# Optimization experiments

Hardware: AMD Instinct MI355X
Metric: run time of the kernel (lower is better)

## Reference

```python
import jax, jax.numpy as jnp
import numpy as np

HID = 256
N_LAYERS = 4
DT = 0.05
EPS = 1e-3
TMAX = 50


def setup_inputs() -> dict:
    key = jax.random.key(0)
    ks = jax.random.split(key, 7)
    B, S, D = 8, 1024, HID
    s1 = 1.0 / np.sqrt(D)      # fan_in = D for w_state / w_input
    s2 = 1.0 / np.sqrt(2 * D)  # fan_in = 2D for tau_gate linear
    x = jax.random.normal(ks[0], (B, S, D), dtype=jnp.float32)
    Ws = jax.random.uniform(ks[1], (N_LAYERS, D, D), jnp.float32, -s1, s1)
    bs = jax.random.uniform(ks[2], (N_LAYERS, D), jnp.float32, -s1, s1)
    Wi = jax.random.uniform(ks[3], (N_LAYERS, D, D), jnp.float32, -s1, s1)
    bi = jax.random.uniform(ks[4], (N_LAYERS, D), jnp.float32, -s1, s1)
    Wt = jax.random.uniform(ks[5], (N_LAYERS, D, 2 * D), jnp.float32, -s2, s2)
    bt = jax.random.uniform(ks[6], (N_LAYERS, D), jnp.float32, -s2, s2)
    return {"x": x, "Ws": Ws, "bs": bs, "Wi": Wi, "bi": bi, "Wt": Wt, "bt": bt}


def _run(x, Ws, bs, Wi, bi, Wt, bt):
    B, S, D = x.shape

    def layer_fn(cur_in, layer):
        h_prev, Ws_i, bs_i, Wi_i, bi_i, Wt_i, bt_i = layer
        combined = jnp.concatenate([cur_in, h_prev], axis=-1)          # [B,S,2D]
        tau = jax.nn.sigmoid(jnp.einsum('bsk,dk->bsd', combined, Wt_i) + bt_i)
        forcing = jnp.tanh(
            jnp.einsum('bsd,ed->bse', h_prev, Ws_i) + bs_i
            + jnp.einsum('bsd,ed->bse', cur_in, Wi_i) + bi_i
        )
        h_new = jnp.clip(h_prev + DT * (-h_prev / (tau + 1e-6) + forcing), -10.0, 10.0)
        delta = jnp.max(jnp.abs(h_new - h_prev))
        return h_new, (h_new, delta)

    @jax.checkpoint
    def step(carry, i):
        states, result, done = carry
        _, (new_states, deltas) = jax.lax.scan(
            layer_fn, x, (states, Ws, bs, Wi, bi, Wt, bt))
        converged = jnp.max(deltas) < EPS
        states = jnp.where(done, states, new_states)
        # torch returns loop index t at the first converging iteration, else TMAX
        result = jnp.where(done | ~converged, result, i)
        done = done | converged
        return (states, result, done), None

    init = (jnp.zeros((N_LAYERS, B, S, D), x.dtype),
            jnp.array(TMAX, jnp.int32),
            jnp.array(False))
    (states, result, _), _ = jax.lax.scan(step, init, jnp.arange(TMAX, dtype=jnp.int32))
    return states[-1], result


def reference(x, Ws, bs, Wi, bi, Wt, bt):
    return _run(x, Ws, bs, Wi, bi, Wt, bt)
```

## Files before the change

### kernel.cpp

```cpp
#include <hip/hip_runtime.h>
#include <math.h>

#define HID 256
#define TWOH 512
#define ROWS 8192
#define NLAYER 4
#define TMAX 50
#define DT 0.05f
#define EPSC 1e-3f

typedef float f32x4 __attribute__((ext_vector_type(4)));
typedef long  long2v __attribute__((ext_vector_type(2)));
typedef unsigned char u8;

__device__ inline u8 f32_to_fp8(float v) {
    return (u8)(__builtin_amdgcn_cvt_pk_fp8_f32(v, v, 0, 0) & 0xff);
}
__device__ inline float fp8_to_f32(u8 b) {
    return __builtin_amdgcn_cvt_f32_fp8((int)b, 0);
}

__global__ void pack_w_kernel(const float* __restrict__ Ws,
                              const float* __restrict__ Wi,
                              const float* __restrict__ Wt,
                              u8* __restrict__ Wf) {
    int e = blockIdx.x * 256 + threadIdx.x;
    int j    = e & 7;
    int h    = (e >> 3) & 1;
    int lane = (e >> 4) & 63;
    int g    = (e >> 10) & 1;
    int ci   = (e >> 11) & 15;
    int wv   = (e >> 15) & 7;
    int L    = (e >> 18);
    int l15  = lane & 15;
    int quad = lane >> 4;
    int d = wv * 32 + h * 16 + l15;
    int k = ci * 32 + quad * 8 + j;
    float v;
    if (g == 0) {
        v = Wt[(size_t)L * HID * TWOH + (size_t)d * TWOH + k];
    } else {
        v = (k < HID) ? Wi[(size_t)L * HID * HID + (size_t)d * HID + k]
                      : Ws[(size_t)L * HID * HID + (size_t)d * HID + (k - HID)];
    }
    Wf[e] = f32_to_fp8(v);
}

__global__ void pack_b_kernel(const float* __restrict__ bs,
                              const float* __restrict__ bi,
                              const float* __restrict__ bt,
                              float* __restrict__ bp) {
    int idx = blockIdx.x * 256 + threadIdx.x;
    int L = idx / TWOH;
    int n = idx % TWOH;
    int d = n >> 1;
    bp[idx] = ((n & 1) == 0) ? bt[L * HID + d]
                             : (bs[L * HID + d] + bi[L * HID + d]);
}

__global__ __launch_bounds__(512, 1) void persistent_kernel(
    const float* __restrict__ x,
    const u8* __restrict__ Wf,
    const float* __restrict__ bp,
    float* __restrict__ deltas,
    float* __restrict__ out)
{
    __shared__ u8 sX[32 * 256];
    __shared__ u8 sH[2][NLAYER][32 * 256];
    __shared__ float2 sBias[NLAYER][256];

    const int tid  = threadIdx.x;
    const int lane = tid & 63;
    const int wv   = tid >> 6;
    const int l15  = lane & 15;
    const int quad = lane >> 4;
    const int w32  = wv * 32;
    const size_t rowbase = (size_t)blockIdx.x * 32;

    #pragma unroll
    for (int it = 0; it < 2; ++it) {
        int s = tid + it * 512;
        int r = s >> 5, seg = s & 31;
        const float* gx = x + (rowbase + r) * HID + seg * 8;
        float4 v0 = *(const float4*)gx;
        float4 v1 = *(const float4*)(gx + 4);
        int lo = __builtin_amdgcn_cvt_pk_fp8_f32(v0.x, v0.y, 0, 0);
        lo     = __builtin_amdgcn_cvt_pk_fp8_f32(v0.z, v0.w, lo, 1);
        int hi = __builtin_amdgcn_cvt_pk_fp8_f32(v1.x, v1.y, 0, 0);
        hi     = __builtin_amdgcn_cvt_pk_fp8_f32(v1.z, v1.w, hi, 1);
        long pk = ((long)(unsigned int)lo) | ((long)hi << 32);
        *(long*)&sX[r * 256 + (seg ^ r) * 8] = pk;
    }
    {
        long* hflat = (long*)&sH[0][0][0];
        #pragma unroll
        for (int it = 0; it < 16; ++it) hflat[tid + it * 512] = 0;
    }
    #pragma unroll
    for (int it = 0; it < 2; ++it) {
        int i = tid + it * 512;
        sBias[i >> 8][i & 255] = *(const float2*)(bp + (i >> 8) * TWOH + 2 * (i & 255));
    }

    __syncthreads();

    #pragma unroll 1
    for (int t = 0; t < TMAX; ++t) {
        const int rs = t & 1, ws = rs ^ 1;
        #pragma unroll 1
        for (int L = 0; L < NLAYER; ++L) {
            const u8* Ahi = &sH[rs][L][0];
            const u8* Alo = (L == 0) ? sX : &sH[ws][L - 1][0];
            u8*       Hout = &sH[ws][L][0];
            const u8* wb = Wf + ((size_t)(L * 8 + wv) << 15) + (size_t)lane * 16;

            f32x4 acc[2][4];
            #pragma unroll
            for (int mt = 0; mt < 2; ++mt)
                #pragma unroll
                for (int n = 0; n < 4; ++n)
                    acc[mt][n] = (f32x4){0.f, 0.f, 0.f, 0.f};

            long2v bb[4][2];
            #pragma unroll
            for (int pi = 0; pi < 4; ++pi)
                #pragma unroll
                for (int g = 0; g < 2; ++g)
                    bb[pi][g] = *(const long2v*)(wb + (size_t)(((8 + pi) * 2 + g) << 10));

            #pragma unroll
            for (int s = 0; s < 16; ++s) {
                const int ci = (s < 8) ? (s + 8) : (s - 8);
                const int p = s & 3;
                if (s == 8) __syncthreads();
                const u8* Asrc = (s < 8) ? Ahi : Alo;
                const int seg = (ci & 7) * 4 + quad;
                long a[2];
                #pragma unroll
                for (int mt = 0; mt < 2; ++mt) {
                    const int row = mt * 16 + l15;
                    a[mt] = *(const long*)&Asrc[row * 256 + (seg ^ row) * 8];
                }
                #pragma unroll
                for (int mt = 0; mt < 2; ++mt)
                    #pragma unroll
                    for (int n = 0; n < 4; ++n)
                        acc[mt][n] = __builtin_amdgcn_mfma_f32_16x16x32_fp8_fp8(
                            a[mt], bb[p][n >> 1][n & 1], acc[mt][n], 0, 0, 0);
                if (s + 4 < 16) {
                    const int nci = (s + 4 < 8) ? (s + 12) : (s - 4);
                    #pragma unroll
                    for (int g = 0; g < 2; ++g)
                        bb[p][g] = *(const long2v*)(wb + (size_t)((nci * 2 + g) << 10));
                }
            }

            float dmax = 0.0f;
            #pragma unroll
            for (int ntp = 0; ntp < 2; ++ntp) {
                const int d = w32 + ntp * 16 + l15;
                const float2 b2 = sBias[L][d];
                const int seg = d >> 3, dlow = d & 7;
                #pragma unroll
                for (int mt = 0; mt < 2; ++mt) {
                    #pragma unroll
                    for (int r = 0; r < 4; ++r) {
                        float tpre = acc[mt][ntp][r]     + b2.x;
                        float fpre = acc[mt][ntp + 2][r] + b2.y;
                        tpre = fminf(30.f, fmaxf(-30.f, tpre));
                        fpre = fminf(15.f, fmaxf(-15.f, fpre));
                        float u   = __expf(-tpre);
                        float den = 1.0f + 1e-6f + 1e-6f * u;
                        float rcp = __builtin_amdgcn_rcpf(den);
                        float e2  = __expf(2.0f * fpre);
                        float r2  = __builtin_amdgcn_rcpf(e2 + 1.0f);
                        float fo  = (e2 - 1.0f) * r2;
                        const int row = mt * 16 + quad * 4 + r;
                        const int idx = row * 256 + (seg ^ row) * 8 + dlow;
                        float h  = fp8_to_f32(Ahi[idx]);
                        float gq = h * (1.0f + u) * rcp;
                        float nv = h + DT * (fo - gq);
                        nv = fminf(10.0f, fmaxf(-10.0f, nv));
                        Hout[idx] = f32_to_fp8(nv);
                        dmax = fmaxf(dmax, fabsf(nv - h));
                    }
                }
            }
            if (L == NLAYER - 1) {
                #pragma unroll
                for (int off = 32; off > 0; off >>= 1)
                    dmax = fmaxf(dmax, __shfl_xor(dmax, off));
                if (lane == 0)
                    atomicMax((unsigned int*)(deltas + t), __float_as_uint(dmax));
            }
        }
    }

    __syncthreads();

    {
        const u8* fin = &sH[((TMAX - 1) & 1) ^ 1][NLAYER - 1][0];
        #pragma unroll
        for (int it = 0; it < 2; ++it) {
            int s = tid + it * 512;
            int r = s >> 5, seg = s & 31;
            long v = *(const long*)&fin[r * 256 + (seg ^ r) * 8];
            int lo = (int)(v & 0xffffffffl);
            int hi = (int)(v >> 32);
            float* go = out + (rowbase + r) * HID + seg * 8;
            float4 o0, o1;
            o0.x = __builtin_amdgcn_cvt_f32_fp8(lo, 0);
            o0.y = __builtin_amdgcn_cvt_f32_fp8(lo, 1);
            o0.z = __builtin_amdgcn_cvt_f32_fp8(lo, 2);
            o0.w = __builtin_amdgcn_cvt_f32_fp8(lo, 3);
            o1.x = __builtin_amdgcn_cvt_f32_fp8(hi, 0);
            o1.y = __builtin_amdgcn_cvt_f32_fp8(hi, 1);
            o1.z = __builtin_amdgcn_cvt_f32_fp8(hi, 2);
            o1.w = __builtin_amdgcn_cvt_f32_fp8(hi, 3);
            *(float4*)go = o0;
            *(float4*)(go + 4) = o1;
        }
    }
}

__global__ void result_kernel(const float* __restrict__ deltas,
                              float* __restrict__ out) {
    if (threadIdx.x == 0) {
        int res = TMAX;
        for (int t = 0; t < TMAX; ++t) {
            if (deltas[t] < EPSC) { res = t; break; }
        }
        out[(size_t)ROWS * HID] = (float)res;
    }
}

extern "C" void kernel_launch(void* const* d_in, const int* in_sizes, int n_in,
                              void* d_out, int out_size, void* d_ws, size_t ws_size,
                              hipStream_t stream) {
    const float* x  = (const float*)d_in[0];
    const float* Ws = (const float*)d_in[1];
    const float* bs = (const float*)d_in[2];
    const float* Wi = (const float*)d_in[3];
    const float* bi = (const float*)d_in[4];
    const float* Wt = (const float*)d_in[5];
    const float* bt = (const float*)d_in[6];
    float* out = (float*)d_out;

    char* p = (char*)d_ws;
    u8*    Wf     = (u8*)p;    p += (size_t)NLAYER * TWOH * TWOH;
    float* bp     = (float*)p; p += (size_t)NLAYER * TWOH * sizeof(float);
    float* deltas = (float*)p; p += 64 * sizeof(float);

    hipMemsetAsync(deltas, 0, 64 * sizeof(float), stream);
    pack_w_kernel<<<(NLAYER * TWOH * TWOH) / 256, 256, 0, stream>>>(Ws, Wi, Wt, Wf);
    pack_b_kernel<<<(NLAYER * TWOH) / 256, 256, 0, stream>>>(bs, bi, bt, bp);

    persistent_kernel<<<256, 512, 0, stream>>>(x, Wf, bp, deltas, out);
    result_kernel<<<1, 64, 0, stream>>>(deltas, out);
}
```

Measured before the change: 1.257 ms.

## Halve rows per block to 16 and launch twice as many blocks

Each persistent block now handles 16 rows instead of 32, so the launch has 512 blocks instead of 256 and each wave issues one M-tile of MFMAs instead of two. The goal is to fill more of the MI355X's CUs, since 256 blocks leaves many idle. In exchange, every block still streams the full fp8 weight set from global/L2 each layer and timestep, which doubles total weight traffic, and weight-load latency is amortised over half as many MFMAs.

```diff
diff --git a/kernel.cpp b/kernel.cpp
--- a/kernel.cpp
+++ b/kernel.cpp
@@ -8,6 +8,7 @@
 #define TMAX 50
 #define DT 0.05f
 #define EPSC 1e-3f
+#define BROW 16
 
 typedef float f32x4 __attribute__((ext_vector_type(4)));
 typedef long  long2v __attribute__((ext_vector_type(2)));
@@ -65,8 +66,8 @@
     float* __restrict__ deltas,
     float* __restrict__ out)
 {
-    __shared__ u8 sX[32 * 256];
-    __shared__ u8 sH[2][NLAYER][32 * 256];
+    __shared__ u8 sX[BROW * 256];
+    __shared__ u8 sH[2][NLAYER][BROW * 256];
     __shared__ float2 sBias[NLAYER][256];
 
     const int tid  = threadIdx.x;
@@ -75,12 +76,10 @@
     const int l15  = lane & 15;
     const int quad = lane >> 4;
     const int w32  = wv * 32;
-    const size_t rowbase = (size_t)blockIdx.x * 32;
-
-    #pragma unroll
-    for (int it = 0; it < 2; ++it) {
-        int s = tid + it * 512;
-        int r = s >> 5, seg = s & 31;
+    const size_t rowbase = (size_t)blockIdx.x * BROW;
+
+    {
+        int r = tid >> 5, seg = tid & 31;
         const float* gx = x + (rowbase + r) * HID + seg * 8;
         float4 v0 = *(const float4*)gx;
         float4 v1 = *(const float4*)(gx + 4);
@@ -94,7 +93,7 @@
     {
         long* hflat = (long*)&sH[0][0][0];
         #pragma unroll
-        for (int it = 0; it < 16; ++it) hflat[tid + it * 512] = 0;
+        for (int it = 0; it < 8; ++it) hflat[tid + it * 512] = 0;
     }
     #pragma unroll
     for (int it = 0; it < 2; ++it) {
@@ -114,12 +113,10 @@
             u8*       Hout = &sH[ws][L][0];
             const u8* wb = Wf + ((size_t)(L * 8 + wv) << 15) + (size_t)lane * 16;
 
-            f32x4 acc[2][4];
-            #pragma unroll
-            for (int mt = 0; mt < 2; ++mt)
-                #pragma unroll
-                for (int n = 0; n < 4; ++n)
-                    acc[mt][n] = (f32x4){0.f, 0.f, 0.f, 0.f};
+            f32x4 acc[4];
+            #pragma unroll
+            for (int n = 0; n < 4; ++n)
+                acc[n] = (f32x4){0.f, 0.f, 0.f, 0.f};
 
             long2v bb[4][2];
             #pragma unroll
@@ -135,18 +132,11 @@
                 if (s == 8) __syncthreads();
                 const u8* Asrc = (s < 8) ? Ahi : Alo;
                 const int seg = (ci & 7) * 4 + quad;
-                long a[2];
-                #pragma unroll
-                for (int mt = 0; mt < 2; ++mt) {
-                    const int row = mt * 16 + l15;
-                    a[mt] = *(const long*)&Asrc[row * 256 + (seg ^ row) * 8];
-                }
-                #pragma unroll
-                for (int mt = 0; mt < 2; ++mt)
-                    #pragma unroll
-                    for (int n = 0; n < 4; ++n)
-                        acc[mt][n] = __builtin_amdgcn_mfma_f32_16x16x32_fp8_fp8(
-                            a[mt], bb[p][n >> 1][n & 1], acc[mt][n], 0, 0, 0);
+                long a = *(const long*)&Asrc[l15 * 256 + (seg ^ l15) * 8];
+                #pragma unroll
+                for (int n = 0; n < 4; ++n)
+                    acc[n] = __builtin_amdgcn_mfma_f32_16x16x32_fp8_fp8(
+                        a, bb[p][n >> 1][n & 1], acc[n], 0, 0, 0);
                 if (s + 4 < 16) {
                     const int nci = (s + 4 < 8) ? (s + 12) : (s - 4);
                     #pragma unroll
@@ -162,28 +152,25 @@
                 const float2 b2 = sBias[L][d];
                 const int seg = d >> 3, dlow = d & 7;
                 #pragma unroll
-                for (int mt = 0; mt < 2; ++mt) {
-                    #pragma unroll
-                    for (int r = 0; r < 4; ++r) {
-                        float tpre = acc[mt][ntp][r]     + b2.x;
-                        float fpre = acc[mt][ntp + 2][r] + b2.y;
-                        tpre = fminf(30.f, fmaxf(-30.f, tpre));
-                        fpre = fminf(15.f, fmaxf(-15.f, fpre));
-                        float u   = __expf(-tpre);
-                        float den = 1.0f + 1e-6f + 1e-6f * u;
-                        float rcp = __builtin_amdgcn_rcpf(den);
-                        float e2  = __expf(2.0f * fpre);
-                        float r2  = __builtin_amdgcn_rcpf(e2 + 1.0f);
-                        float fo  = (e2 - 1.0f) * r2;
-                        const int row = mt * 16 + quad * 4 + r;
-                        const int idx = row * 256 + (seg ^ row) * 8 + dlow;
-                        float h  = fp8_to_f32(Ahi[idx]);
-                        float gq = h * (1.0f + u) * rcp;
-                        float nv = h + DT * (fo - gq);
-                        nv = fminf(10.0f, fmaxf(-10.0f, nv));
-                        Hout[idx] = f32_to_fp8(nv);
-                        dmax = fmaxf(dmax, fabsf(nv - h));
-                    }
+                for (int r = 0; r < 4; ++r) {
+                    float tpre = acc[ntp][r]     + b2.x;
+                    float fpre = acc[ntp + 2][r] + b2.y;
+                    tpre = fminf(30.f, fmaxf(-30.f, tpre));
+                    fpre = fminf(15.f, fmaxf(-15.f, fpre));
+                    float u   = __expf(-tpre);
+                    float den = 1.0f + 1e-6f + 1e-6f * u;
+                    float rcp = __builtin_amdgcn_rcpf(den);
+                    float e2  = __expf(2.0f * fpre);
+                    float r2  = __builtin_amdgcn_rcpf(e2 + 1.0f);
+                    float fo  = (e2 - 1.0f) * r2;
+                    const int row = quad * 4 + r;
+                    const int idx = row * 256 + (seg ^ row) * 8 + dlow;
+                    float h  = fp8_to_f32(Ahi[idx]);
+                    float gq = h * (1.0f + u) * rcp;
+                    float nv = h + DT * (fo - gq);
+                    nv = fminf(10.0f, fmaxf(-10.0f, nv));
+                    Hout[idx] = f32_to_fp8(nv);
+                    dmax = fmaxf(dmax, fabsf(nv - h));
                 }
             }
             if (L == NLAYER - 1) {
@@ -200,26 +187,22 @@
 
     {
         const u8* fin = &sH[((TMAX - 1) & 1) ^ 1][NLAYER - 1][0];
-        #pragma unroll
-        for (int it = 0; it < 2; ++it) {
-            int s = tid + it * 512;
-            int r = s >> 5, seg = s & 31;
-            long v = *(const long*)&fin[r * 256 + (seg ^ r) * 8];
-            int lo = (int)(v & 0xffffffffl);
-            int hi = (int)(v >> 32);
-            float* go = out + (rowbase + r) * HID + seg * 8;
-            float4 o0, o1;
-            o0.x = __builtin_amdgcn_cvt_f32_fp8(lo, 0);
-            o0.y = __builtin_amdgcn_cvt_f32_fp8(lo, 1);
-            o0.z = __builtin_amdgcn_cvt_f32_fp8(lo, 2);
-            o0.w = __builtin_amdgcn_cvt_f32_fp8(lo, 3);
-            o1.x = __builtin_amdgcn_cvt_f32_fp8(hi, 0);
-            o1.y = __builtin_amdgcn_cvt_f32_fp8(hi, 1);
-            o1.z = __builtin_amdgcn_cvt_f32_fp8(hi, 2);
-            o1.w = __builtin_amdgcn_cvt_f32_fp8(hi, 3);
-            *(float4*)go = o0;
-            *(float4*)(go + 4) = o1;
-        }
+        int r = tid >> 5, seg = tid & 31;
+        long v = *(const long*)&fin[r * 256 + (seg ^ r) * 8];
+        int lo = (int)(v & 0xffffffffl);
+        int hi = (int)(v >> 32);
+        float* go = out + (rowbase + r) * HID + seg * 8;
+        float4 o0, o1;
+        o0.x = __builtin_amdgcn_cvt_f32_fp8(lo, 0);
+        o0.y = __builtin_amdgcn_cvt_f32_fp8(lo, 1);
+        o0.z = __builtin_amdgcn_cvt_f32_fp8(lo, 2);
+        o0.w = __builtin_amdgcn_cvt_f32_fp8(lo, 3);
+        o1.x = __builtin_amdgcn_cvt_f32_fp8(hi, 0);
+        o1.y = __builtin_amdgcn_cvt_f32_fp8(hi, 1);
+        o1.z = __builtin_amdgcn_cvt_f32_fp8(hi, 2);
+        o1.w = __builtin_amdgcn_cvt_f32_fp8(hi, 3);
+        *(float4*)go = o0;
+        *(float4*)(go + 4) = o1;
     }
 }
 
@@ -255,6 +238,6 @@
     pack_w_kernel<<<(NLAYER * TWOH * TWOH) / 256, 256, 0, stream>>>(Ws, Wi, Wt, Wf);
     pack_b_kernel<<<(NLAYER * TWOH) / 256, 256, 0, stream>>>(bs, bi, bt, bp);
 
-    persistent_kernel<<<256, 512, 0, stream>>>(x, Wf, bp, deltas, out);
+    persistent_kernel<<<ROWS / BROW, 512, 0, stream>>>(x, Wf, bp, deltas, out);
     result_kernel<<<1, 64, 0, stream>>>(deltas, out);
 }
```

Result: slower. 1.726 ms (+37.3%).
